# Kernel optimization log

Hardware: AMD Instinct MI355X
Metric: run time of the kernel (lower is better)

Reference implementation:

```python
import jax, jax.numpy as jnp
import numpy as np

B, S, D, U = 8, 2048, 512, 512
L0, L1 = 128, 128  # limit_context (left, right)


def setup_inputs() -> dict:
    key = jax.random.key(0)
    ks = jax.random.split(key, 7)
    scale = 1.0 / np.sqrt(D).astype(np.float32)
    return {
        "x": jax.random.normal(ks[0], (B, S, D), dtype=jnp.float32),
        "Wq": jax.random.normal(ks[1], (D, U), dtype=jnp.float32) * scale,
        "Wk": jax.random.normal(ks[2], (D, U), dtype=jnp.float32) * scale,
        "Wv": jax.random.normal(ks[3], (D, U), dtype=jnp.float32) * scale,
        "bq": jnp.zeros((U,), dtype=jnp.float32),
        "bk": jnp.zeros((U,), dtype=jnp.float32),
        "bv": jnp.zeros((U,), dtype=jnp.float32),
    }


def reference(x, Wq, Wk, Wv, bq, bk, bv):
    # Linear projections for query / key / value (shared input x)
    q = x @ Wq + bq  # [B,S,U]
    k = x @ Wk + bk  # [B,S,U]
    v = x @ Wv + bv  # [B,S,U]

    inv_sqrt_dv = jnp.float32(1.0 / np.sqrt(U))
    scores = jnp.einsum("bqd,bkd->bqk", q, k) * inv_sqrt_dv  # [B,S,S]

    # Sliding-window mask: key j visible to query i iff i-L0 <= j <= i+L1.
    # Equivalent to the original per-step softmax over values[:, start:end].
    i = jnp.arange(S)[:, None]
    j = jnp.arange(S)[None, :]
    window = (j >= i - L0) & (j <= i + L1)  # [S,S]
    neg_inf = jnp.finfo(scores.dtype).min
    scores = jnp.where(window[None], scores, neg_inf)

    attn = jax.nn.softmax(scores, axis=-1)  # [B,S,S]
    return jnp.einsum("bqk,bkd->bqd", attn, v)  # [B,S,U]
```

## Files before the change

### kernel.cpp

```cpp
#include <hip/hip_runtime.h>

#define BATCH 8
#define S_LEN 2048
#define DDIM 512
#define UDIM 512
#define WIN_L 128
#define WIN_R 128
#define KP 520
#define VP 40
#define PP 296

typedef _Float16 f16;
typedef __attribute__((ext_vector_type(8))) _Float16 f16x8;
typedef __attribute__((ext_vector_type(4))) _Float16 f16x4;
typedef __attribute__((ext_vector_type(4))) float f32x4;

__device__ __forceinline__ void gload_lds16(const void* g, void* l) {
  __builtin_amdgcn_global_load_lds((const __attribute__((address_space(1))) void*)g,
                                   (__attribute__((address_space(3))) void*)l, 16, 0, 0);
}

__global__ void prep(const float* __restrict__ x, const float* __restrict__ Wq,
                     const float* __restrict__ Wk, const float* __restrict__ Wv,
                     f16* __restrict__ xb, f16* __restrict__ WT) {
  __shared__ float t[32][33];
  int bid = blockIdx.x;
  if (bid < 8192) {
    int i = (bid * 256 + threadIdx.x) * 4;
    float4 v = *(const float4*)(x + i);
    f16x4 o;
    o[0] = (f16)v.x; o[1] = (f16)v.y; o[2] = (f16)v.z; o[3] = (f16)v.w;
    *(f16x4*)(xb + i) = o;
  } else {
    int id = bid - 8192;
    int zx = id & 15, zy = (id >> 4) & 15, zz = id >> 8;
    const float* W = zz == 0 ? Wq : (zz == 1 ? Wk : Wv);
    f16* WTz = WT + (size_t)zz * DDIM * UDIM;
    int tx = threadIdx.x & 31, ty = threadIdx.x >> 5;
    int n0 = zx * 32, k0 = zy * 32;
    for (int i = 0; i < 4; i++) {
      int r = ty * 4 + i;
      t[r][tx] = W[(size_t)(k0 + r) * UDIM + n0 + tx];
    }
    __syncthreads();
    for (int i = 0; i < 4; i++) {
      int r = ty * 4 + i;
      WTz[(size_t)(n0 + r) * DDIM + k0 + tx] = (f16)t[tx][r];
    }
  }
}

__global__ __launch_bounds__(256, 3) void gemm_qkv(
    const f16* __restrict__ X, const f16* __restrict__ WT,
    const float* __restrict__ bq, const float* __restrict__ bk, const float* __restrict__ bv,
    f16* __restrict__ QKV, f16* __restrict__ VT) {
  int z = blockIdx.z;
  const f16* WTz = WT + (size_t)z * DDIM * UDIM;
  const float* bias = z == 0 ? bq : (z == 1 ? bk : bv);
  f16* out = QKV + (size_t)z * (BATCH * S_LEN) * UDIM;

  __shared__ f16 Al[2][128 * 32];
  __shared__ f16 Bl[2][128 * 32];

  int tid = threadIdx.x, wv = tid >> 6, ln = tid & 63;
  int m0 = blockIdx.x * 128, n0 = blockIdx.y * 128;
  int wm = (wv >> 1) * 64, wn = (wv & 1) * 64;
  int lm = ln & 15, lq = ln >> 4;
  int srow = ln >> 2, scol = (ln & 3) * 8;

  f32x4 acc[4][4];
#pragma unroll
  for (int mt = 0; mt < 4; mt++)
    for (int nt = 0; nt < 4; nt++)
      for (int r = 0; r < 4; r++) acc[mt][nt][r] = 0.f;

  for (int k0 = 0; k0 < DDIM; k0 += 64) {
#pragma unroll
    for (int half = 0; half < 2; half++) {
      int r0 = half * 64 + wv * 16;
#pragma unroll
      for (int c = 0; c < 2; c++) {
        gload_lds16(X + (size_t)(m0 + r0 + srow) * DDIM + k0 + c * 32 + scol, &Al[c][r0 * 32]);
        gload_lds16(WTz + (size_t)(n0 + r0 + srow) * DDIM + k0 + c * 32 + scol, &Bl[c][r0 * 32]);
      }
    }
    __syncthreads();
#pragma unroll
    for (int c = 0; c < 2; c++) {
      f16x8 af[4], bfr[4];
#pragma unroll
      for (int mt = 0; mt < 4; mt++) af[mt] = *(const f16x8*)&Al[c][(wm + mt * 16 + lm) * 32 + lq * 8];
#pragma unroll
      for (int nt = 0; nt < 4; nt++) bfr[nt] = *(const f16x8*)&Bl[c][(wn + nt * 16 + lm) * 32 + lq * 8];
#pragma unroll
      for (int mt = 0; mt < 4; mt++)
#pragma unroll
        for (int nt = 0; nt < 4; nt++)
          acc[mt][nt] = __builtin_amdgcn_mfma_f32_16x16x32_f16(af[mt], bfr[nt], acc[mt][nt], 0, 0, 0);
    }
    __syncthreads();
  }

  if (z == 2) {
#pragma unroll
    for (int mt = 0; mt < 4; mt++)
#pragma unroll
      for (int nt = 0; nt < 4; nt++) {
        int col = n0 + wn + nt * 16 + lm;
        float bv_ = bias[col];
        int row0 = m0 + wm + mt * 16 + lq * 4;
        int bb = row0 >> 11, ss = row0 & 2047;
        f16x4 o;
        for (int r = 0; r < 4; r++) o[r] = (f16)(acc[mt][nt][r] + bv_);
        *(f16x4*)&VT[((size_t)bb * UDIM + col) * S_LEN + ss] = o;
      }
  } else {
#pragma unroll
    for (int mt = 0; mt < 4; mt++)
#pragma unroll
      for (int nt = 0; nt < 4; nt++) {
        int col = n0 + wn + nt * 16 + lm;
        float bv_ = bias[col];
        for (int r = 0; r < 4; r++) {
          int row = m0 + wm + mt * 16 + lq * 4 + r;
          out[(size_t)row * UDIM + col] = (f16)(acc[mt][nt][r] + bv_);
        }
      }
  }
}

__global__ __launch_bounds__(256, 2) void attn(
    const f16* __restrict__ Q, const f16* __restrict__ K, const f16* __restrict__ VT,
    float* __restrict__ out) {
  __shared__ __align__(16) char ubuf[VP * 512 * 2];
  __shared__ f16 Pb[32 * PP];
  __shared__ float wmax[2][32], wsum[2][32];
  f16* Kl = (f16*)ubuf;
  f16* Vl = (f16*)ubuf;

  int tid = threadIdx.x, wv = tid >> 6, ln = tid & 63;
  int lm = ln & 15, lq = ln >> 4;
  int b = blockIdx.x, q0 = blockIdx.y * 32;
  int rh = wv >> 1, kh = wv & 1;
  const size_t base = (size_t)b * S_LEN;
  const int strip0 = q0 - WIN_L;
  const int t_lo = strip0 < 0 ? (-strip0) >> 5 : 0;
  int t_hi = (S_LEN - strip0) >> 5; if (t_hi > 9) t_hi = 9;

  f16x8 qf[16];
  {
    const f16* qrow = Q + (base + q0 + rh * 16 + lm) * (size_t)DDIM + lq * 8;
#pragma unroll
    for (int kk = 0; kk < 16; kk++) qf[kk] = *(const f16x8*)(qrow + kk * 32);
  }

  f32x4 sacc[9];
#pragma unroll
  for (int s = 0; s < 9; s++)
    for (int r = 0; r < 4; r++) sacc[s][r] = 0.f;

#pragma unroll
  for (int s = 0; s < 9; s++) {
    if (s >= t_lo && s < t_hi) {
      int j0 = strip0 + s * 32;
#pragma unroll
      for (int i = 0; i < 8; i++) {
        int row = wv * 8 + i;
        int key = j0 + row;
        int kc = key < 0 ? 0 : (key > S_LEN - 1 ? S_LEN - 1 : key);
        gload_lds16(K + (base + kc) * (size_t)DDIM + ln * 8, &Kl[row * KP]);
      }
      __syncthreads();
      f32x4 s0, s1;
      for (int r = 0; r < 4; r++) { s0[r] = 0.f; s1[r] = 0.f; }
#pragma unroll
      for (int kk = 0; kk < 16; kk += 2) {
        f16x8 b0 = *(const f16x8*)&Kl[(kh * 16 + lm) * KP + kk * 32 + lq * 8];
        f16x8 b1 = *(const f16x8*)&Kl[(kh * 16 + lm) * KP + (kk + 1) * 32 + lq * 8];
        s0 = __builtin_amdgcn_mfma_f32_16x16x32_f16(qf[kk], b0, s0, 0, 0, 0);
        s1 = __builtin_amdgcn_mfma_f32_16x16x32_f16(qf[kk + 1], b1, s1, 0, 0, 0);
      }
      for (int r = 0; r < 4; r++) sacc[s][r] = s0[r] + s1[r];
      __syncthreads();
    }
  }

  const float scale = 0.044194173824159216f;
  float mx[4] = {-1e30f, -1e30f, -1e30f, -1e30f};
#pragma unroll
  for (int s = 0; s < 9; s++) {
    int kj = strip0 + s * 32 + kh * 16 + lm;
#pragma unroll
    for (int r = 0; r < 4; r++) {
      int qi = q0 + rh * 16 + lq * 4 + r;
      float v = sacc[s][r] * scale;
      bool ok = (kj >= 0) && (kj < S_LEN) && (kj >= qi - WIN_L) && (kj <= qi + WIN_R);
      v = ok ? v : -1e30f;
      sacc[s][r] = v;
      mx[r] = fmaxf(mx[r], v);
    }
  }
#pragma unroll
  for (int r = 0; r < 4; r++) {
    mx[r] = fmaxf(mx[r], __shfl_xor(mx[r], 1));
    mx[r] = fmaxf(mx[r], __shfl_xor(mx[r], 2));
    mx[r] = fmaxf(mx[r], __shfl_xor(mx[r], 4));
    mx[r] = fmaxf(mx[r], __shfl_xor(mx[r], 8));
  }
  if (lm == 0) {
#pragma unroll
    for (int r = 0; r < 4; r++) wmax[kh][rh * 16 + lq * 4 + r] = mx[r];
  }
  __syncthreads();

  float mrow[4], sum[4] = {0.f, 0.f, 0.f, 0.f};
#pragma unroll
  for (int r = 0; r < 4; r++) {
    int row = rh * 16 + lq * 4 + r;
    mrow[r] = fmaxf(wmax[0][row], wmax[1][row]);
  }
#pragma unroll
  for (int s = 0; s < 9; s++) {
#pragma unroll
    for (int r = 0; r < 4; r++) {
      float p = __expf(sacc[s][r] - mrow[r]);
      sum[r] += p;
      Pb[(rh * 16 + lq * 4 + r) * PP + s * 32 + kh * 16 + lm] = (f16)p;
    }
  }
#pragma unroll
  for (int r = 0; r < 4; r++) {
    sum[r] += __shfl_xor(sum[r], 1);
    sum[r] += __shfl_xor(sum[r], 2);
    sum[r] += __shfl_xor(sum[r], 4);
    sum[r] += __shfl_xor(sum[r], 8);
  }
  if (lm == 0) {
#pragma unroll
    for (int r = 0; r < 4; r++) wsum[kh][rh * 16 + lq * 4 + r] = sum[r];
  }
  __syncthreads();

  f32x4 oacc[2][8];
#pragma unroll
  for (int mt = 0; mt < 2; mt++)
    for (int nt = 0; nt < 8; nt++)
      for (int r = 0; r < 4; r++) oacc[mt][nt][r] = 0.f;

  int vu = (tid >> 2), vc4 = tid & 3;
  const f16* vsrc = VT + ((size_t)b * UDIM + vu) * S_LEN;
  f16x8 vreg[8];
  {
    int j0 = strip0 + t_lo * 32;
    int key = j0 + vc4 * 8;
    int kc = key < 0 ? 0 : (key > S_LEN - 8 ? S_LEN - 8 : key);
#pragma unroll
    for (int i = 0; i < 8; i++) vreg[i] = *(const f16x8*)(vsrc + (size_t)(i * 64) * S_LEN + kc);
  }

  for (int t = t_lo; t < t_hi; t++) {
#pragma unroll
    for (int i = 0; i < 8; i++) *(f16x8*)&Vl[(i * 64 + vu) * VP + vc4 * 8] = vreg[i];
    __syncthreads();
    if (t + 1 < t_hi) {
      int j0 = strip0 + (t + 1) * 32;
      int key = j0 + vc4 * 8;
      int kc = key < 0 ? 0 : (key > S_LEN - 8 ? S_LEN - 8 : key);
#pragma unroll
      for (int i = 0; i < 8; i++) vreg[i] = *(const f16x8*)(vsrc + (size_t)(i * 64) * S_LEN + kc);
    }
    f16x8 pf0 = *(const f16x8*)&Pb[lm * PP + t * 32 + lq * 8];
    f16x8 pf1 = *(const f16x8*)&Pb[(16 + lm) * PP + t * 32 + lq * 8];
#pragma unroll
    for (int nt = 0; nt < 8; nt++) {
      f16x8 vvf = *(const f16x8*)&Vl[(wv * 128 + nt * 16 + lm) * VP + lq * 8];
      oacc[0][nt] = __builtin_amdgcn_mfma_f32_16x16x32_f16(pf0, vvf, oacc[0][nt], 0, 0, 0);
      oacc[1][nt] = __builtin_amdgcn_mfma_f32_16x16x32_f16(pf1, vvf, oacc[1][nt], 0, 0, 0);
    }
    __syncthreads();
  }

  float linv[2][4];
#pragma unroll
  for (int mt = 0; mt < 2; mt++)
    for (int r = 0; r < 4; r++) {
      int row = mt * 16 + lq * 4 + r;
      linv[mt][r] = 1.0f / (wsum[0][row] + wsum[1][row]);
    }
#pragma unroll
  for (int mt = 0; mt < 2; mt++)
    for (int nt = 0; nt < 8; nt++)
      for (int r = 0; r < 4; r++) {
        int row = q0 + mt * 16 + lq * 4 + r;
        int col = wv * 128 + nt * 16 + lm;
        out[(base + row) * (size_t)UDIM + col] = oacc[mt][nt][r] * linv[mt][r];
      }
}

extern "C" void kernel_launch(void* const* d_in, const int* in_sizes, int n_in,
                              void* d_out, int out_size, void* d_ws, size_t ws_size,
                              hipStream_t stream) {
  const float* x  = (const float*)d_in[0];
  const float* Wq = (const float*)d_in[1];
  const float* Wk = (const float*)d_in[2];
  const float* Wv = (const float*)d_in[3];
  const float* bq = (const float*)d_in[4];
  const float* bk = (const float*)d_in[5];
  const float* bv = (const float*)d_in[6];
  float* out = (float*)d_out;

  char* ws = (char*)d_ws;
  const size_t XB_BYTES  = (size_t)BATCH * S_LEN * DDIM * 2;
  const size_t WT_BYTES  = (size_t)3 * DDIM * UDIM * 2;
  const size_t QKV_BYTES = (size_t)3 * BATCH * S_LEN * UDIM * 2;
  f16* xb  = (f16*)ws;
  f16* WT  = (f16*)(ws + XB_BYTES);
  f16* QKV = (f16*)(ws + XB_BYTES + WT_BYTES);
  f16* VT  = (f16*)(ws + XB_BYTES + WT_BYTES + QKV_BYTES);

  prep<<<8192 + 768, 256, 0, stream>>>(x, Wq, Wk, Wv, xb, WT);
  gemm_qkv<<<dim3(128, 4, 3), 256, 0, stream>>>(xb, WT, bq, bk, bv, QKV, VT);
  attn<<<dim3(BATCH, S_LEN / 32), 256, 0, stream>>>(
      QKV, QKV + (size_t)BATCH * S_LEN * UDIM, VT, out);
}
```

Before: 155.9 us.

## Fuse fp32-to-fp16 input conversion into QKV GEMM with register prefetch and XCD remap

Removes the separate pass that converted x to fp16. The QKV GEMM now loads fp32 x tiles straight into registers, converts them and stores them to LDS, prefetching the next K tile during the MFMA loop. The grid is flattened and remapped so the 12 blocks sharing an M tile land on the same XCD, which should keep the repeated fp32 x reads in that XCD's L2. In exchange, x is reread at twice the width, register pressure rises, and the A-tile load becomes synchronous through VGPRs instead of a direct global-to-LDS copy.

Measured after the change: 153.7 us. About the same (-1.4%).

```diff
diff --git a/kernel.cpp b/kernel.cpp
--- a/kernel.cpp
+++ b/kernel.cpp
@@ -20,41 +20,36 @@
                                    (__attribute__((address_space(3))) void*)l, 16, 0, 0);
 }
 
-__global__ void prep(const float* __restrict__ x, const float* __restrict__ Wq,
-                     const float* __restrict__ Wk, const float* __restrict__ Wv,
-                     f16* __restrict__ xb, f16* __restrict__ WT) {
+__global__ void prep(const float* __restrict__ Wq, const float* __restrict__ Wk,
+                     const float* __restrict__ Wv, f16* __restrict__ WT) {
   __shared__ float t[32][33];
-  int bid = blockIdx.x;
-  if (bid < 8192) {
-    int i = (bid * 256 + threadIdx.x) * 4;
-    float4 v = *(const float4*)(x + i);
-    f16x4 o;
-    o[0] = (f16)v.x; o[1] = (f16)v.y; o[2] = (f16)v.z; o[3] = (f16)v.w;
-    *(f16x4*)(xb + i) = o;
-  } else {
-    int id = bid - 8192;
-    int zx = id & 15, zy = (id >> 4) & 15, zz = id >> 8;
-    const float* W = zz == 0 ? Wq : (zz == 1 ? Wk : Wv);
-    f16* WTz = WT + (size_t)zz * DDIM * UDIM;
-    int tx = threadIdx.x & 31, ty = threadIdx.x >> 5;
-    int n0 = zx * 32, k0 = zy * 32;
-    for (int i = 0; i < 4; i++) {
-      int r = ty * 4 + i;
-      t[r][tx] = W[(size_t)(k0 + r) * UDIM + n0 + tx];
-    }
-    __syncthreads();
-    for (int i = 0; i < 4; i++) {
-      int r = ty * 4 + i;
-      WTz[(size_t)(n0 + r) * DDIM + k0 + tx] = (f16)t[tx][r];
-    }
+  int id = blockIdx.x;
+  int zx = id & 15, zy = (id >> 4) & 15, zz = id >> 8;
+  const float* W = zz == 0 ? Wq : (zz == 1 ? Wk : Wv);
+  f16* WTz = WT + (size_t)zz * DDIM * UDIM;
+  int tx = threadIdx.x & 31, ty = threadIdx.x >> 5;
+  int n0 = zx * 32, k0 = zy * 32;
+  for (int i = 0; i < 4; i++) {
+    int r = ty * 4 + i;
+    t[r][tx] = W[(size_t)(k0 + r) * UDIM + n0 + tx];
+  }
+  __syncthreads();
+  for (int i = 0; i < 4; i++) {
+    int r = ty * 4 + i;
+    WTz[(size_t)(n0 + r) * DDIM + k0 + tx] = (f16)t[tx][r];
   }
 }
 
 __global__ __launch_bounds__(256, 3) void gemm_qkv(
-    const f16* __restrict__ X, const f16* __restrict__ WT,
+    const float* __restrict__ X32, const f16* __restrict__ WT,
     const float* __restrict__ bq, const float* __restrict__ bk, const float* __restrict__ bv,
     f16* __restrict__ QKV, f16* __restrict__ VT) {
-  int z = blockIdx.z;
+  int g = blockIdx.x;
+  int xcd = g & 7, j = g >> 3;
+  int m_blk = xcd * 16 + (j & 15);
+  int rest = j >> 4;
+  int ny = rest & 3, z = rest >> 2;
+
   const f16* WTz = WT + (size_t)z * DDIM * UDIM;
   const float* bias = z == 0 ? bq : (z == 1 ? bk : bv);
   f16* out = QKV + (size_t)z * (BATCH * S_LEN) * UDIM;
@@ -63,10 +58,11 @@
   __shared__ f16 Bl[2][128 * 32];
 
   int tid = threadIdx.x, wv = tid >> 6, ln = tid & 63;
-  int m0 = blockIdx.x * 128, n0 = blockIdx.y * 128;
+  int m0 = m_blk * 128, n0 = ny * 128;
   int wm = (wv >> 1) * 64, wn = (wv & 1) * 64;
   int lm = ln & 15, lq = ln >> 4;
   int srow = ln >> 2, scol = (ln & 3) * 8;
+  int arow = ln >> 2, acol = (ln & 3) * 8;
 
   f32x4 acc[4][4];
 #pragma unroll
@@ -74,17 +70,47 @@
     for (int nt = 0; nt < 4; nt++)
       for (int r = 0; r < 4; r++) acc[mt][nt][r] = 0.f;
 
+  float4 ap[2][2][2];
+#pragma unroll
+  for (int c = 0; c < 2; c++)
+#pragma unroll
+    for (int h = 0; h < 2; h++) {
+      const float* p = X32 + (size_t)(m0 + wv * 32 + h * 16 + arow) * DDIM + c * 32 + (ln & 3) * 8;
+      ap[c][h][0] = *(const float4*)p;
+      ap[c][h][1] = *(const float4*)(p + 4);
+    }
+
   for (int k0 = 0; k0 < DDIM; k0 += 64) {
+#pragma unroll
+    for (int c = 0; c < 2; c++)
+#pragma unroll
+      for (int h = 0; h < 2; h++) {
+        float4 p0 = ap[c][h][0], p1 = ap[c][h][1];
+        f16x8 o;
+        o[0] = (f16)p0.x; o[1] = (f16)p0.y; o[2] = (f16)p0.z; o[3] = (f16)p0.w;
+        o[4] = (f16)p1.x; o[5] = (f16)p1.y; o[6] = (f16)p1.z; o[7] = (f16)p1.w;
+        *(f16x8*)&Al[c][(wv * 32 + h * 16 + arow) * 32 + acol] = o;
+      }
 #pragma unroll
     for (int half = 0; half < 2; half++) {
       int r0 = half * 64 + wv * 16;
 #pragma unroll
-      for (int c = 0; c < 2; c++) {
-        gload_lds16(X + (size_t)(m0 + r0 + srow) * DDIM + k0 + c * 32 + scol, &Al[c][r0 * 32]);
+      for (int c = 0; c < 2; c++)
         gload_lds16(WTz + (size_t)(n0 + r0 + srow) * DDIM + k0 + c * 32 + scol, &Bl[c][r0 * 32]);
-      }
     }
     __syncthreads();
+
+    if (k0 + 64 < DDIM) {
+#pragma unroll
+      for (int c = 0; c < 2; c++)
+#pragma unroll
+        for (int h = 0; h < 2; h++) {
+          const float* p = X32 + (size_t)(m0 + wv * 32 + h * 16 + arow) * DDIM + (k0 + 64) + c * 32 + (ln & 3) * 8;
+          ap[c][h][0] = *(const float4*)p;
+          ap[c][h][1] = *(const float4*)(p + 4);
+        }
+    }
+
 #pragma unroll
     for (int c = 0; c < 2; c++) {
       f16x8 af[4], bfr[4];
@@ -310,16 +336,14 @@
   float* out = (float*)d_out;
 
   char* ws = (char*)d_ws;
-  const size_t XB_BYTES  = (size_t)BATCH * S_LEN * DDIM * 2;
   const size_t WT_BYTES  = (size_t)3 * DDIM * UDIM * 2;
   const size_t QKV_BYTES = (size_t)3 * BATCH * S_LEN * UDIM * 2;
-  f16* xb  = (f16*)ws;
-  f16* WT  = (f16*)(ws + XB_BYTES);
-  f16* QKV = (f16*)(ws + XB_BYTES + WT_BYTES);
-  f16* VT  = (f16*)(ws + XB_BYTES + WT_BYTES + QKV_BYTES);
-
-  prep<<<8192 + 768, 256, 0, stream>>>(x, Wq, Wk, Wv, xb, WT);
-  gemm_qkv<<<dim3(128, 4, 3), 256, 0, stream>>>(xb, WT, bq, bk, bv, QKV, VT);
+  f16* WT  = (f16*)ws;
+  f16* QKV = (f16*)(ws + WT_BYTES);
+  f16* VT  = (f16*)(ws + WT_BYTES + QKV_BYTES);
+
+  prep<<<768, 256, 0, stream>>>(Wq, Wk, Wv, WT);
+  gemm_qkv<<<1536, 256, 0, stream>>>(x, WT, bq, bk, bv, QKV, VT);
   attn<<<dim3(BATCH, S_LEN / 32), 256, 0, stream>>>(
       QKV, QKV + (size_t)BATCH * S_LEN * UDIM, VT, out);
 }
```
